# Kernel optimization log

Hardware: AMD Instinct MI355X
Metric: run time of the kernel (lower is better)

## Reference

```python
import jax, jax.numpy as jnp
import numpy as np

B, I, H = 16384, 1024, 1024
W_SCALE = 0.03  # keep gate pre-activations in a sane range (mimics small init)


def setup_inputs() -> dict:
    key = jax.random.key(0)
    ks = jax.random.split(key, 7)
    return {
        "x": jax.random.normal(ks[0], (B, I), dtype=jnp.float32),
        "c": jax.random.normal(ks[1], (B, H), dtype=jnp.float32),
        "h": jax.random.normal(ks[2], (B, H), dtype=jnp.float32),
        # gate order along axis 0: f (forget), i (input), k (cell cand), o (output)
        "Wx": jax.random.normal(ks[3], (4, H, I), dtype=jnp.float32) * W_SCALE,
        "bx": jax.random.normal(ks[4], (4, H), dtype=jnp.float32) * W_SCALE,
        "Wh": jax.random.normal(ks[5], (4, H, H), dtype=jnp.float32) * W_SCALE,
        "bh": jax.random.normal(ks[6], (4, H), dtype=jnp.float32) * W_SCALE,
    }


def reference(x, c, h, Wx, bx, Wh, bh):
    # Fused equivalent of the 8 tiny nn.Linear calls: one stacked GEMM each
    # for input->hidden and hidden->hidden. pre: [B, 4, H]
    pre = (jnp.einsum('bi,ghi->bgh', x, Wx)
           + jnp.einsum('bk,ghk->bgh', h, Wh)
           + bx[None] + bh[None])
    f = jax.nn.sigmoid(pre[:, 0])   # forget gate (w1/r1)
    i = jax.nn.sigmoid(pre[:, 1])   # input gate  (w2/r2)
    k = jnp.tanh(pre[:, 2])         # cell candidate (w3/r3)
    o = jax.nn.sigmoid(pre[:, 3])   # output gate (w4/r4)
    c_new = f * c + i * k
    h_new = o * jnp.tanh(c_new)
    return (o, c_new, h_new)
```

## Files before the change

### kernel.cpp

```cpp
#include <hip/hip_runtime.h>
#include <hip/hip_bf16.h>
#include <cstdint>

#define DI __device__ __forceinline__

typedef __attribute__((ext_vector_type(4))) float f32x4;
typedef __attribute__((ext_vector_type(8))) short bf16x8;

static constexpr int B_ = 16384, I_ = 1024, H_ = 1024;
static constexpr int M = B_;
static constexpr int N = 4 * H_;
static constexpr int K = I_ + H_;
static constexpr int NT = K / 64;

static constexpr size_t OFF_A  = 0;
static constexpr size_t OFF_W  = OFF_A + (size_t)M * K * 2;
static constexpr size_t OFF_BI = OFF_W + (size_t)N * K * 2;

DI unsigned short f2bf(float f) {
    union { float f; unsigned u; } v; v.f = f;
    unsigned r = v.u + 0x7FFFu + ((v.u >> 16) & 1u);
    return (unsigned short)(r >> 16);
}

__global__ void cvt_kernel(const float* __restrict__ x, const float* __restrict__ h,
                           const float* __restrict__ Wx, const float* __restrict__ Wh,
                           unsigned short* __restrict__ A, unsigned short* __restrict__ W)
{
    long tid = (long)blockIdx.x * blockDim.x + threadIdx.x;
    long row = tid >> 9;
    int  col = (int)(tid & 511) * 4;
    const float* src;
    unsigned short* dst;
    if (row < M) {
        src = (col < I_) ? x + (size_t)row * I_ + col
                         : h + (size_t)row * H_ + (col - I_);
        dst = A + (size_t)row * K + col;
    } else {
        int r = (int)(row - M);
        int gate = (r >> 4) & 3;
        int hcol = ((r >> 6) << 4) | (r & 15);
        int srow = gate * H_ + hcol;
        src = (col < I_) ? Wx + (size_t)srow * I_ + col
                         : Wh + (size_t)srow * H_ + (col - I_);
        dst = W + (size_t)r * K + col;
    }
    float4 v = *(const float4*)src;
    ushort4 o;
    o.x = f2bf(v.x); o.y = f2bf(v.y); o.z = f2bf(v.z); o.w = f2bf(v.w);
    *(ushort4*)dst = o;
}

__global__ void bias_kernel(const float* __restrict__ bx, const float* __restrict__ bh,
                            float* __restrict__ bias)
{
    int r = blockIdx.x * blockDim.x + threadIdx.x;
    if (r < N) {
        int gate = (r >> 4) & 3;
        int hcol = ((r >> 6) << 4) | (r & 15);
        int s = gate * H_ + hcol;
        bias[r] = bx[s] + bh[s];
    }
}

DI void stage_half(const unsigned short* __restrict__ g, int grow0, int kcol,
                   unsigned short* ldsbase, int tid)
{
    const int w    = tid >> 6, lane = tid & 63;
    const int rsub = (w << 3) + (lane >> 3);
    const int kk   = kcol + (((lane & 7) ^ (lane >> 3)) << 3);
#pragma unroll
    for (int l = 0; l < 2; ++l) {
        const unsigned short* gp = g + (size_t)(grow0 + (l << 6) + rsub) * K + kk;
        unsigned short* lp = ldsbase + (((l << 6) + (w << 3)) << 6);
        __builtin_amdgcn_global_load_lds(
            (const __attribute__((address_space(1))) void*)gp,
            (__attribute__((address_space(3))) void*)lp, 16, 0, 0);
    }
}

DI bf16x8 ldfrag(const unsigned short* tile, int row, int ks, int lane)
{
    const int sl = ((ks << 2) + (lane >> 4)) ^ (lane & 7);
    return *(const bf16x8*)(tile + (row << 6) + (sl << 3));
}

DI float sigf(float v) { return 1.f / (1.f + __expf(-v)); }
DI float tanhfast(float v) {
    float vc = fminf(fmaxf(v, -15.f), 15.f);
    float e  = __expf(2.f * vc);
    return (e - 1.f) / (e + 1.f);
}

#define MFMA_QUAD(MH, N0)                                                     \
  _Pragma("unroll") for (int ks_ = 0; ks_ < 2; ++ks_)                         \
  _Pragma("unroll") for (int m_ = 0; m_ < 4; ++m_)                            \
  _Pragma("unroll") for (int dn_ = 0; dn_ < 2; ++dn_)                         \
    acc[(MH)*4 + m_][(N0) + dn_] = __builtin_amdgcn_mfma_f32_16x16x32_bf16(   \
        a[m_][ks_], b[(N0) + dn_][ks_], acc[(MH)*4 + m_][(N0) + dn_], 0, 0, 0);

#define PHASE_MFMA(MH, N0)                                                    \
    __builtin_amdgcn_s_barrier();                                             \
    asm volatile("s_waitcnt lgkmcnt(0)");                                     \
    __builtin_amdgcn_s_setprio(1);                                            \
    MFMA_QUAD(MH, N0);                                                        \
    __builtin_amdgcn_s_setprio(0);                                            \
    __builtin_amdgcn_s_barrier();

__global__ __launch_bounds__(512, 2) void gemm_lstm(
    const unsigned short* __restrict__ Abf, const unsigned short* __restrict__ Wbf,
    const float* __restrict__ bias, const float* __restrict__ c,
    float* __restrict__ out)
{
    __shared__ __align__(16) unsigned short sh[65536];

    const int tid  = threadIdx.x;
    const int lane = tid & 63;
    const int wid  = tid >> 6;
    const int wr   = wid >> 2;
    const int wc   = wid & 3;

    const int bid  = blockIdx.x;
    const int wg   = ((bid & 7) << 7) | (bid >> 3);
    const int nbk  = wg & 15, mbk = wg >> 4;
    const int brow = mbk << 8, bcol = nbk << 8;

    const int l15  = lane & 15;
    const int rA0  = (wr << 7) + l15;
    const int rB0  = (wc << 6) + l15;

    f32x4 acc[8][4];
#pragma unroll
    for (int i = 0; i < 8; ++i)
#pragma unroll
        for (int j = 0; j < 4; ++j) acc[i][j] = f32x4{0.f, 0.f, 0.f, 0.f};
    bf16x8 a[4][2], b[4][2];

    {
        unsigned short* A0 = sh;
        unsigned short* B0 = sh + 16384;
        unsigned short* A1 = sh + 32768;
        unsigned short* B1 = sh + 32768 + 16384;
        stage_half(Abf, brow,       0, A0,        tid);
        stage_half(Abf, brow + 128, 0, A0 + 8192, tid);
        stage_half(Wbf, bcol,       0, B0,        tid);
        stage_half(Wbf, bcol + 128, 0, B0 + 8192, tid);
        stage_half(Wbf, bcol,      64, B1,        tid);
        stage_half(Wbf, bcol + 128,64, B1 + 8192, tid);
        stage_half(Abf, brow,      64, A1,        tid);
        asm volatile("s_waitcnt vmcnt(6)" ::: "memory");
        __builtin_amdgcn_s_barrier();
    }

    for (int t = 0; t < NT; ++t) {
        const int q = t & 1;
        unsigned short* curA = sh + q * 32768;
        unsigned short* curB = curA + 16384;
        unsigned short* oA   = sh + (q ^ 1) * 32768;
        const int k1 = ((t + 1) & 31) << 6;
        const int k2 = ((t + 2) & 31) << 6;

        stage_half(Abf, brow + 128, k1, oA + 8192, tid);
#pragma unroll
        for (int m = 0; m < 4; ++m)
#pragma unroll
            for (int ks = 0; ks < 2; ++ks)
                a[m][ks] = ldfrag(curA, rA0 + m * 16, ks, lane);
#pragma unroll
        for (int n = 0; n < 2; ++n)
#pragma unroll
            for (int ks = 0; ks < 2; ++ks)
                b[n][ks] = ldfrag(curB, rB0 + n * 16, ks, lane);
        PHASE_MFMA(0, 0);

#pragma unroll
        for (int n = 2; n < 4; ++n)
#pragma unroll
            for (int ks = 0; ks < 2; ++ks)
                b[n][ks] = ldfrag(curB, rB0 + n * 16, ks, lane);
        PHASE_MFMA(0, 2);

        stage_half(Wbf, bcol, k2, curB, tid);
#pragma unroll
        for (int m = 0; m < 4; ++m)
#pragma unroll
            for (int ks = 0; ks < 2; ++ks)
                a[m][ks] = ldfrag(curA, rA0 + 64 + m * 16, ks, lane);
        PHASE_MFMA(1, 2);

        stage_half(Wbf, bcol + 128, k2, curB + 8192, tid);
        stage_half(Abf, brow, k2, curA, tid);
        asm volatile("s_waitcnt vmcnt(6)" ::: "memory");
        PHASE_MFMA(1, 0);
    }

    asm volatile("s_waitcnt vmcnt(0)" ::: "memory");

    const int hcol  = (((nbk << 2) + wc) << 4) + l15;
    const int crow0 = brow + (wr << 7) + ((lane >> 4) << 2);
    const int cb0   = bcol + (wc << 6) + l15;
    const float bs0 = bias[cb0];
    const float bs1 = bias[cb0 + 16];
    const float bs2 = bias[cb0 + 32];
    const float bs3 = bias[cb0 + 48];
    const size_t P  = (size_t)B_ * H_;
#pragma unroll
    for (int mf = 0; mf < 8; ++mf) {
#pragma unroll
        for (int j = 0; j < 4; ++j) {
            const int row = crow0 + mf * 16 + j;
            const size_t base = (size_t)row * H_ + hcol;
            float fg = sigf(acc[mf][0][j] + bs0);
            float ig = sigf(acc[mf][1][j] + bs1);
            float kg = tanhfast(acc[mf][2][j] + bs2);
            float og = sigf(acc[mf][3][j] + bs3);
            float cv = c[base];
            float cn = fg * cv + ig * kg;
            float hn = og * tanhfast(cn);
            out[base]         = og;
            out[P + base]     = cn;
            out[2 * P + base] = hn;
        }
    }
}

extern "C" void kernel_launch(void* const* d_in, const int* in_sizes, int n_in,
                              void* d_out, int out_size, void* d_ws, size_t ws_size,
                              hipStream_t stream)
{
    const float* x  = (const float*)d_in[0];
    const float* c  = (const float*)d_in[1];
    const float* h  = (const float*)d_in[2];
    const float* Wx = (const float*)d_in[3];
    const float* bx = (const float*)d_in[4];
    const float* Wh = (const float*)d_in[5];
    const float* bh = (const float*)d_in[6];

    unsigned short* Abf  = (unsigned short*)((char*)d_ws + OFF_A);
    unsigned short* Wbf  = (unsigned short*)((char*)d_ws + OFF_W);
    float*          bias = (float*)((char*)d_ws + OFF_BI);
    float*          out  = (float*)d_out;

    cvt_kernel<<<40960, 256, 0, stream>>>(x, h, Wx, Wh, Abf, Wbf);
    bias_kernel<<<16, 256, 0, stream>>>(bx, bh, bias);
    gemm_lstm<<<(M / 256) * (N / 256), 512, 0, stream>>>(
        Abf, Wbf, bias, c, out);
}
```

Measured before the change: 339.4 us.

## Double block to 1024 threads with 64x64 per-wave tiles and simple double-buffering

After: 362.1 us. +6.7%, slower.

```diff
diff --git a/kernel.cpp b/kernel.cpp
--- a/kernel.cpp
+++ b/kernel.cpp
@@ -63,20 +63,18 @@
     }
 }
 
-DI void stage_half(const unsigned short* __restrict__ g, int grow0, int kcol,
-                   unsigned short* ldsbase, int tid)
-{
-    const int w    = tid >> 6, lane = tid & 63;
+DI void stage_half16(const unsigned short* __restrict__ g, int grow0, int kcol,
+                     unsigned short* ldsbase, int tid)
+{
+    const int w    = tid >> 6;
+    const int lane = tid & 63;
     const int rsub = (w << 3) + (lane >> 3);
     const int kk   = kcol + (((lane & 7) ^ (lane >> 3)) << 3);
-#pragma unroll
-    for (int l = 0; l < 2; ++l) {
-        const unsigned short* gp = g + (size_t)(grow0 + (l << 6) + rsub) * K + kk;
-        unsigned short* lp = ldsbase + (((l << 6) + (w << 3)) << 6);
-        __builtin_amdgcn_global_load_lds(
-            (const __attribute__((address_space(1))) void*)gp,
-            (__attribute__((address_space(3))) void*)lp, 16, 0, 0);
-    }
+    const unsigned short* gp = g + (size_t)(grow0 + rsub) * K + kk;
+    unsigned short* lp = ldsbase + ((w << 3) << 6);
+    __builtin_amdgcn_global_load_lds(
+        (const __attribute__((address_space(1))) void*)gp,
+        (__attribute__((address_space(3))) void*)lp, 16, 0, 0);
 }
 
 DI bf16x8 ldfrag(const unsigned short* tile, int row, int ks, int lane)
@@ -92,22 +90,20 @@
     return (e - 1.f) / (e + 1.f);
 }
 
-#define MFMA_QUAD(MH, N0)                                                     \
-  _Pragma("unroll") for (int ks_ = 0; ks_ < 2; ++ks_)                         \
-  _Pragma("unroll") for (int m_ = 0; m_ < 4; ++m_)                            \
-  _Pragma("unroll") for (int dn_ = 0; dn_ < 2; ++dn_)                         \
-    acc[(MH)*4 + m_][(N0) + dn_] = __builtin_amdgcn_mfma_f32_16x16x32_bf16(   \
-        a[m_][ks_], b[(N0) + dn_][ks_], acc[(MH)*4 + m_][(N0) + dn_], 0, 0, 0);
-
-#define PHASE_MFMA(MH, N0)                                                    \
+#define PHASE_MFMA8(M0)                                                       \
     __builtin_amdgcn_s_barrier();                                             \
     asm volatile("s_waitcnt lgkmcnt(0)");                                     \
     __builtin_amdgcn_s_setprio(1);                                            \
-    MFMA_QUAD(MH, N0);                                                        \
+    _Pragma("unroll") for (int n_ = 0; n_ < 4; ++n_)                          \
+        acc[M0][n_] = __builtin_amdgcn_mfma_f32_16x16x32_bf16(                \
+            a2[0], b4[n_], acc[M0][n_], 0, 0, 0);                             \
+    _Pragma("unroll") for (int n_ = 0; n_ < 4; ++n_)                          \
+        acc[(M0) + 1][n_] = __builtin_amdgcn_mfma_f32_16x16x32_bf16(          \
+            a2[1], b4[n_], acc[(M0) + 1][n_], 0, 0, 0);                       \
     __builtin_amdgcn_s_setprio(0);                                            \
     __builtin_amdgcn_s_barrier();
 
-__global__ __launch_bounds__(512, 2) void gemm_lstm(
+__global__ __launch_bounds__(1024, 4) void gemm_lstm(
     const unsigned short* __restrict__ Abf, const unsigned short* __restrict__ Wbf,
     const float* __restrict__ bias, const float* __restrict__ c,
     float* __restrict__ out)
@@ -126,29 +122,22 @@
     const int brow = mbk << 8, bcol = nbk << 8;
 
     const int l15  = lane & 15;
-    const int rA0  = (wr << 7) + l15;
+    const int rA0  = (wr << 6) + l15;
     const int rB0  = (wc << 6) + l15;
 
-    f32x4 acc[8][4];
-#pragma unroll
-    for (int i = 0; i < 8; ++i)
+    f32x4 acc[4][4];
+#pragma unroll
+    for (int i = 0; i < 4; ++i)
 #pragma unroll
         for (int j = 0; j < 4; ++j) acc[i][j] = f32x4{0.f, 0.f, 0.f, 0.f};
-    bf16x8 a[4][2], b[4][2];
+    bf16x8 a2[2], b4[4];
 
     {
-        unsigned short* A0 = sh;
-        unsigned short* B0 = sh + 16384;
-        unsigned short* A1 = sh + 32768;
-        unsigned short* B1 = sh + 32768 + 16384;
-        stage_half(Abf, brow,       0, A0,        tid);
-        stage_half(Abf, brow + 128, 0, A0 + 8192, tid);
-        stage_half(Wbf, bcol,       0, B0,        tid);
-        stage_half(Wbf, bcol + 128, 0, B0 + 8192, tid);
-        stage_half(Wbf, bcol,      64, B1,        tid);
-        stage_half(Wbf, bcol + 128,64, B1 + 8192, tid);
-        stage_half(Abf, brow,      64, A1,        tid);
-        asm volatile("s_waitcnt vmcnt(6)" ::: "memory");
+        stage_half16(Abf, brow,       0, sh,         tid);
+        stage_half16(Abf, brow + 128, 0, sh + 8192,  tid);
+        stage_half16(Wbf, bcol,       0, sh + 16384, tid);
+        stage_half16(Wbf, bcol + 128, 0, sh + 24576, tid);
+        asm volatile("s_waitcnt vmcnt(0)" ::: "memory");
         __builtin_amdgcn_s_barrier();
     }
 
@@ -156,48 +145,40 @@
         const int q = t & 1;
         unsigned short* curA = sh + q * 32768;
         unsigned short* curB = curA + 16384;
-        unsigned short* oA   = sh + (q ^ 1) * 32768;
-        const int k1 = ((t + 1) & 31) << 6;
-        const int k2 = ((t + 2) & 31) << 6;
-
-        stage_half(Abf, brow + 128, k1, oA + 8192, tid);
-#pragma unroll
-        for (int m = 0; m < 4; ++m)
-#pragma unroll
-            for (int ks = 0; ks < 2; ++ks)
-                a[m][ks] = ldfrag(curA, rA0 + m * 16, ks, lane);
-#pragma unroll
-        for (int n = 0; n < 2; ++n)
-#pragma unroll
-            for (int ks = 0; ks < 2; ++ks)
-                b[n][ks] = ldfrag(curB, rB0 + n * 16, ks, lane);
-        PHASE_MFMA(0, 0);
-
-#pragma unroll
-        for (int n = 2; n < 4; ++n)
-#pragma unroll
-            for (int ks = 0; ks < 2; ++ks)
-                b[n][ks] = ldfrag(curB, rB0 + n * 16, ks, lane);
-        PHASE_MFMA(0, 2);
-
-        stage_half(Wbf, bcol, k2, curB, tid);
-#pragma unroll
-        for (int m = 0; m < 4; ++m)
-#pragma unroll
-            for (int ks = 0; ks < 2; ++ks)
-                a[m][ks] = ldfrag(curA, rA0 + 64 + m * 16, ks, lane);
-        PHASE_MFMA(1, 2);
-
-        stage_half(Wbf, bcol + 128, k2, curB + 8192, tid);
-        stage_half(Abf, brow, k2, curA, tid);
-        asm volatile("s_waitcnt vmcnt(6)" ::: "memory");
-        PHASE_MFMA(1, 0);
-    }
-
-    asm volatile("s_waitcnt vmcnt(0)" ::: "memory");
+        unsigned short* nxtA = sh + (q ^ 1) * 32768;
+        unsigned short* nxtB = nxtA + 16384;
+        const int k1 = (t + 1) << 6;
+
+        if (t + 1 < NT) {
+            stage_half16(Abf, brow,       k1, nxtA,        tid);
+            stage_half16(Abf, brow + 128, k1, nxtA + 8192, tid);
+            stage_half16(Wbf, bcol,       k1, nxtB,        tid);
+            stage_half16(Wbf, bcol + 128, k1, nxtB + 8192, tid);
+        }
+        a2[0] = ldfrag(curA, rA0,      0, lane);
+        a2[1] = ldfrag(curA, rA0 + 16, 0, lane);
+#pragma unroll
+        for (int n = 0; n < 4; ++n) b4[n] = ldfrag(curB, rB0 + n * 16, 0, lane);
+        PHASE_MFMA8(0);
+
+        a2[0] = ldfrag(curA, rA0 + 32, 0, lane);
+        a2[1] = ldfrag(curA, rA0 + 48, 0, lane);
+        PHASE_MFMA8(2);
+
+        a2[0] = ldfrag(curA, rA0,      1, lane);
+        a2[1] = ldfrag(curA, rA0 + 16, 1, lane);
+#pragma unroll
+        for (int n = 0; n < 4; ++n) b4[n] = ldfrag(curB, rB0 + n * 16, 1, lane);
+        PHASE_MFMA8(0);
+
+        a2[0] = ldfrag(curA, rA0 + 32, 1, lane);
+        a2[1] = ldfrag(curA, rA0 + 48, 1, lane);
+        asm volatile("s_waitcnt vmcnt(0)" ::: "memory");
+        PHASE_MFMA8(2);
+    }
 
     const int hcol  = (((nbk << 2) + wc) << 4) + l15;
-    const int crow0 = brow + (wr << 7) + ((lane >> 4) << 2);
+    const int crow0 = brow + (wr << 6) + ((lane >> 4) << 2);
     const int cb0   = bcol + (wc << 6) + l15;
     const float bs0 = bias[cb0];
     const float bs1 = bias[cb0 + 16];
@@ -205,7 +186,7 @@
     const float bs3 = bias[cb0 + 48];
     const size_t P  = (size_t)B_ * H_;
 #pragma unroll
-    for (int mf = 0; mf < 8; ++mf) {
+    for (int mf = 0; mf < 4; ++mf) {
 #pragma unroll
         for (int j = 0; j < 4; ++j) {
             const int row = crow0 + mf * 16 + j;
@@ -243,6 +224,6 @@
 
     cvt_kernel<<<40960, 256, 0, stream>>>(x, h, Wx, Wh, Abf, Wbf);
     bias_kernel<<<16, 256, 0, stream>>>(bx, bh, bias);
-    gemm_lstm<<<(M / 256) * (N / 256), 512, 0, stream>>>(
+    gemm_lstm<<<(M / 256) * (N / 256), 1024, 0, stream>>>(
         Abf, Wbf, bias, c, out);
 }
```

## Replace 8-wave ping-pong phased pipeline with simple double-buffered loop

Applied to the files above, without the earlier changes.

New measurement: 335.5 us. Within noise of the previous version (-1.2%).

```diff
diff --git a/kernel.cpp b/kernel.cpp
--- a/kernel.cpp
+++ b/kernel.cpp
@@ -92,21 +92,6 @@
     return (e - 1.f) / (e + 1.f);
 }
 
-#define MFMA_QUAD(MH, N0)                                                     \
-  _Pragma("unroll") for (int ks_ = 0; ks_ < 2; ++ks_)                         \
-  _Pragma("unroll") for (int m_ = 0; m_ < 4; ++m_)                            \
-  _Pragma("unroll") for (int dn_ = 0; dn_ < 2; ++dn_)                         \
-    acc[(MH)*4 + m_][(N0) + dn_] = __builtin_amdgcn_mfma_f32_16x16x32_bf16(   \
-        a[m_][ks_], b[(N0) + dn_][ks_], acc[(MH)*4 + m_][(N0) + dn_], 0, 0, 0);
-
-#define PHASE_MFMA(MH, N0)                                                    \
-    __builtin_amdgcn_s_barrier();                                             \
-    asm volatile("s_waitcnt lgkmcnt(0)");                                     \
-    __builtin_amdgcn_s_setprio(1);                                            \
-    MFMA_QUAD(MH, N0);                                                        \
-    __builtin_amdgcn_s_setprio(0);                                            \
-    __builtin_amdgcn_s_barrier();
-
 __global__ __launch_bounds__(512, 2) void gemm_lstm(
     const unsigned short* __restrict__ Abf, const unsigned short* __restrict__ Wbf,
     const float* __restrict__ bias, const float* __restrict__ c,
@@ -137,18 +122,11 @@
     bf16x8 a[4][2], b[4][2];
 
     {
-        unsigned short* A0 = sh;
-        unsigned short* B0 = sh + 16384;
-        unsigned short* A1 = sh + 32768;
-        unsigned short* B1 = sh + 32768 + 16384;
-        stage_half(Abf, brow,       0, A0,        tid);
-        stage_half(Abf, brow + 128, 0, A0 + 8192, tid);
-        stage_half(Wbf, bcol,       0, B0,        tid);
-        stage_half(Wbf, bcol + 128, 0, B0 + 8192, tid);
-        stage_half(Wbf, bcol,      64, B1,        tid);
-        stage_half(Wbf, bcol + 128,64, B1 + 8192, tid);
-        stage_half(Abf, brow,      64, A1,        tid);
-        asm volatile("s_waitcnt vmcnt(6)" ::: "memory");
+        stage_half(Abf, brow,       0, sh,         tid);
+        stage_half(Abf, brow + 128, 0, sh + 8192,  tid);
+        stage_half(Wbf, bcol,       0, sh + 16384, tid);
+        stage_half(Wbf, bcol + 128, 0, sh + 24576, tid);
+        asm volatile("s_waitcnt vmcnt(0)" ::: "memory");
         __builtin_amdgcn_s_barrier();
     }
 
@@ -156,45 +134,53 @@
         const int q = t & 1;
         unsigned short* curA = sh + q * 32768;
         unsigned short* curB = curA + 16384;
-        unsigned short* oA   = sh + (q ^ 1) * 32768;
+        unsigned short* nxtA = sh + (q ^ 1) * 32768;
+        unsigned short* nxtB = nxtA + 16384;
         const int k1 = ((t + 1) & 31) << 6;
-        const int k2 = ((t + 2) & 31) << 6;
-
-        stage_half(Abf, brow + 128, k1, oA + 8192, tid);
+
+        stage_half(Abf, brow,       k1, nxtA,        tid);
+        stage_half(Abf, brow + 128, k1, nxtA + 8192, tid);
+        stage_half(Wbf, bcol,       k1, nxtB,        tid);
+        stage_half(Wbf, bcol + 128, k1, nxtB + 8192, tid);
+
+#pragma unroll
+        for (int n = 0; n < 4; ++n)
+#pragma unroll
+            for (int ks = 0; ks < 2; ++ks)
+                b[n][ks] = ldfrag(curB, rB0 + n * 16, ks, lane);
 #pragma unroll
         for (int m = 0; m < 4; ++m)
 #pragma unroll
             for (int ks = 0; ks < 2; ++ks)
                 a[m][ks] = ldfrag(curA, rA0 + m * 16, ks, lane);
-#pragma unroll
-        for (int n = 0; n < 2; ++n)
-#pragma unroll
-            for (int ks = 0; ks < 2; ++ks)
-                b[n][ks] = ldfrag(curB, rB0 + n * 16, ks, lane);
-        PHASE_MFMA(0, 0);
-
-#pragma unroll
-        for (int n = 2; n < 4; ++n)
-#pragma unroll
-            for (int ks = 0; ks < 2; ++ks)
-                b[n][ks] = ldfrag(curB, rB0 + n * 16, ks, lane);
-        PHASE_MFMA(0, 2);
-
-        stage_half(Wbf, bcol, k2, curB, tid);
+
+#pragma unroll
+        for (int ks = 0; ks < 2; ++ks)
+#pragma unroll
+            for (int m = 0; m < 4; ++m)
+#pragma unroll
+                for (int n = 0; n < 4; ++n)
+                    acc[m][n] = __builtin_amdgcn_mfma_f32_16x16x32_bf16(
+                        a[m][ks], b[n][ks], acc[m][n], 0, 0, 0);
+
 #pragma unroll
         for (int m = 0; m < 4; ++m)
 #pragma unroll
             for (int ks = 0; ks < 2; ++ks)
                 a[m][ks] = ldfrag(curA, rA0 + 64 + m * 16, ks, lane);
-        PHASE_MFMA(1, 2);
-
-        stage_half(Wbf, bcol + 128, k2, curB + 8192, tid);
-        stage_half(Abf, brow, k2, curA, tid);
-        asm volatile("s_waitcnt vmcnt(6)" ::: "memory");
-        PHASE_MFMA(1, 0);
-    }
-
-    asm volatile("s_waitcnt vmcnt(0)" ::: "memory");
+
+#pragma unroll
+        for (int ks = 0; ks < 2; ++ks)
+#pragma unroll
+            for (int m = 0; m < 4; ++m)
+#pragma unroll
+                for (int n = 0; n < 4; ++n)
+                    acc[4 + m][n] = __builtin_amdgcn_mfma_f32_16x16x32_bf16(
+                        a[m][ks], b[n][ks], acc[4 + m][n], 0, 0, 0);
+
+        asm volatile("s_waitcnt vmcnt(0)" ::: "memory");
+        __builtin_amdgcn_s_barrier();
+    }
 
     const int hcol  = (((nbk << 2) + wc) << 4) + l15;
     const int crow0 = brow + (wr << 7) + ((lane >> 4) << 2);
```
